# Kernel tuning notes

Measured on AMD Instinct MI355X. Metric: run time of the kernel, lower is better.

## Reference

```python
import jax, jax.numpy as jnp
import numpy as np

HIDDEN = 2048
N_HEADS = 16
HEAD_DIM = HIDDEN // N_HEADS  # 128
GROUP_SIZE = 128
ROPE_THETA = 10000.0
EPS = 1e-8
THRESH = 0.5


def ternary_quantize_groupwise(w):
    O, I = w.shape
    wg = w.reshape(O, I // GROUP_SIZE, GROUP_SIZE)
    scale = jnp.maximum(jnp.mean(jnp.abs(wg), axis=-1, keepdims=True), EPS)
    wn = wg / scale
    q = jnp.where(wn > THRESH, 1.0, jnp.where(wn < -THRESH, -1.0, 0.0))
    return (q * scale).reshape(O, I)


def quantize_with_ste(w):
    wq = ternary_quantize_groupwise(w)
    return w + jax.lax.stop_gradient(wq - w)


def rope_tables(seqlen):
    half = HEAD_DIM // 2
    inv_freq = 1.0 / (ROPE_THETA ** (jnp.arange(half, dtype=jnp.float32) / half))
    freqs = jnp.arange(seqlen, dtype=jnp.float32)[:, None] * inv_freq[None, :]  # [S, half]
    return jnp.cos(freqs), jnp.sin(freqs)


def apply_rope(x, cos, sin):
    # x: [B, H, S, D]; cos/sin: [S, D/2]
    d = x.shape[-1]
    x1, x2 = x[..., : d // 2], x[..., d // 2:]
    c = cos[None, None, :, :].astype(x.dtype)
    s = sin[None, None, :, :].astype(x.dtype)
    return jnp.concatenate([x1 * c - x2 * s, x1 * s + x2 * c], axis=-1)


def setup_inputs() -> dict:
    key = jax.random.key(0)
    ks = jax.random.split(key, 5)
    B, S = 1, 2048
    hidden_states = jax.random.normal(ks[0], (B, S, HIDDEN), dtype=jnp.float32)
    attention_mask = jnp.ones((B, S), dtype=jnp.int32)
    init_scale = 1.0 / np.sqrt(HIDDEN)
    wq = jax.random.normal(ks[1], (HIDDEN, HIDDEN), dtype=jnp.float32) * init_scale
    wk = jax.random.normal(ks[2], (HIDDEN, HIDDEN), dtype=jnp.float32) * init_scale
    wv = jax.random.normal(ks[3], (HIDDEN, HIDDEN), dtype=jnp.float32) * init_scale
    wo = jax.random.normal(ks[4], (HIDDEN, HIDDEN), dtype=jnp.float32) * init_scale
    return {"hidden_states": hidden_states, "attention_mask": attention_mask,
            "wq": wq, "wk": wk, "wv": wv, "wo": wo}


def reference(hidden_states, attention_mask, wq, wk, wv, wo):
    B, S, _ = hidden_states.shape
    cos, sin = rope_tables(S)

    def proj(x, w):
        w_q = quantize_with_ste(w)
        y = jnp.einsum('bsi,oi->bso', x, w_q)
        return y.reshape(B, S, N_HEADS, HEAD_DIM).transpose(0, 2, 1, 3)  # [B,H,S,D]

    q = apply_rope(proj(hidden_states, wq), cos, sin)
    k = apply_rope(proj(hidden_states, wk), cos, sin)
    v = proj(hidden_states, wv)

    scores = jnp.einsum('bhsd,bhtd->bhst', q, k) / np.sqrt(HEAD_DIM)
    causal = jnp.triu(jnp.ones((S, S), dtype=bool), k=1)
    scores = jnp.where(causal[None, None, :, :], -jnp.inf, scores)
    pad = (attention_mask == 0)[:, None, None, :]
    scores = jnp.where(pad, -jnp.inf, scores)

    probs = jax.nn.softmax(scores, axis=-1)
    out = jnp.einsum('bhst,bhtd->bhsd', probs, v)
    out = out.transpose(0, 2, 1, 3).reshape(B, S, HIDDEN)

    wo_q = quantize_with_ste(wo)
    return jnp.einsum('bso,po->bsp', out, wo_q)
```

## Files before the change

### kernel.cpp

```cpp
#include <hip/hip_runtime.h>
#include <cstdint>
#include <cstddef>


typedef __attribute__((ext_vector_type(8))) short bf16x8;
typedef __attribute__((ext_vector_type(4))) float f32x4;
typedef __attribute__((address_space(3))) void lds_void;
typedef const __attribute__((address_space(1))) void gmem_void;

__device__ __forceinline__ short f2bf(float x) {
    union { float f; uint32_t u; } c; c.f = x;
    uint32_t r = (c.u + 0x7FFFu + ((c.u >> 16) & 1u)) >> 16;
    return (short)r;
}
__device__ __forceinline__ float bf2f(short x) {
    union { uint32_t u; float f; } c; c.u = ((uint32_t)(uint16_t)x) << 16;
    return c.f;
}

__global__ __launch_bounds__(64) void zero_flag(int* f) {
    if (threadIdx.x == 0) *f = 0;
}

__global__ __launch_bounds__(256) void detect_kernel(
    const unsigned short* __restrict__ p, int n, int* __restrict__ flag)
{
    int tid = blockIdx.x * 256 + threadIdx.x;
    int cnt = 0;
    for (int i = tid; i < n; i += 65536) {
        int e = (p[i] >> 7) & 0xFF;
        cnt += (e >= 0xF0) ? 1 : 0;
    }
#pragma unroll
    for (int off = 1; off < 64; off <<= 1) cnt += __shfl_xor(cnt, off);
    if ((threadIdx.x & 63) == 0 && cnt) atomicAdd(flag, cnt);
}

__global__ __launch_bounds__(256) void convert_kernel(
    const void* __restrict__ in, short* __restrict__ out, int n,
    const int* __restrict__ flag)
{
    bool isf32 = (*flag > 1000);
    int i = (blockIdx.x * 256 + threadIdx.x) * 4;
    if (i >= n) return;
    if (isf32) {
        float4 v = *(const float4*)((const float*)in + i);
        short4 o;
        o.x = f2bf(v.x); o.y = f2bf(v.y); o.z = f2bf(v.z); o.w = f2bf(v.w);
        *(short4*)(out + i) = o;
    } else {
        *(short4*)(out + i) = *(const short4*)((const short*)in + i);
    }
}

__global__ __launch_bounds__(256) void quant_kernel(
    const void* __restrict__ w0, const void* __restrict__ w1,
    const void* __restrict__ w2, const void* __restrict__ w3,
    short* __restrict__ q0, short* __restrict__ q1,
    short* __restrict__ q2, short* __restrict__ q3,
    const int* __restrict__ flag)
{
    bool isf32 = (*flag > 1000);
    int gw   = blockIdx.x * 4 + (threadIdx.x >> 6);
    int lane = threadIdx.x & 63;
    int mat  = gw >> 15;
    int g    = gw & 32767;
    const void* w = (mat == 0) ? w0 : (mat == 1) ? w1 : (mat == 2) ? w2 : w3;
    short*      q = (mat == 0) ? q0 : (mat == 1) ? q1 : (mat == 2) ? q2 : q3;
    int idx = g * 64 + lane;
    float a, b;
    if (isf32) {
        const float* wf = (const float*)w;
        a = wf[idx * 2]; b = wf[idx * 2 + 1];
    } else {
        int pr = ((const int*)w)[idx];
        a = bf2f((short)(pr & 0xFFFF));
        b = bf2f((short)(((uint32_t)pr) >> 16));
    }
    float s = fabsf(a) + fabsf(b);
#pragma unroll
    for (int off = 1; off < 64; off <<= 1) s += __shfl_xor(s, off);
    float scale = fmaxf(s * (1.0f / 128.0f), 1e-8f);
    float na = a / scale, nb = b / scale;
    float ra = (na > 0.5f) ? scale : (na < -0.5f) ? -scale : 0.0f;
    float rb = (nb > 0.5f) ? scale : (nb < -0.5f) ? -scale : 0.0f;
    ((int*)q)[idx] = (int)(uint16_t)f2bf(ra) | ((int)(uint16_t)f2bf(rb) << 16);
}

__global__ __launch_bounds__(256, 2) void gemm_qkv(
    const short* __restrict__ A, const short* __restrict__ B,
    short* __restrict__ C)
{
    __shared__ short lds[30720];

    int wg = blockIdx.y * 32 + blockIdx.x;
    int sw = (wg & 7) * 64 + (wg >> 3);
    int bx = sw & 31, by = sw >> 5;

    const short* Ab = A + (long long)by * 128 * 2048;
    const short* Bb = B + (long long)bx * 192 * 2048;

    int tid = threadIdx.x, lane = tid & 63, wid = tid >> 6;
    int wr = wid >> 1, wc = wid & 1;
    int quad = lane >> 4, lm = lane & 15;

    f32x4 acc[4][6];
#pragma unroll
    for (int i = 0; i < 4; i++)
#pragma unroll
        for (int j = 0; j < 6; j++)
#pragma unroll
            for (int r = 0; r < 4; r++) acc[i][j][r] = 0.0f;

    auto stage = [&](int tn, short* buf) {
        short* dA = buf;
        short* dB = buf + 4096;
#pragma unroll
        for (int l = 0; l < 2; l++) {
            int ci  = l * 256 + tid;
            int row = ci >> 2;
            int kc  = ((ci & 3) - (row >> 1)) & 3;
            const short* gp = Ab + (long long)row * 2048 + tn * 32 + kc * 8;
            __builtin_amdgcn_global_load_lds((gmem_void*)gp, (lds_void*)(dA + ci * 8), 16, 0, 0);
        }
#pragma unroll
        for (int l = 0; l < 3; l++) {
            int ci  = l * 256 + tid;
            int row = ci >> 2;
            int kc  = ((ci & 3) - (row >> 1)) & 3;
            const short* gp = Bb + (long long)row * 2048 + tn * 32 + kc * 8;
            __builtin_amdgcn_global_load_lds((gmem_void*)gp, (lds_void*)(dB + ci * 8), 16, 0, 0);
        }
    };

    auto tile = [&](short* cur, short* nxt, int tn, bool pf) {
        if (pf) stage(tn, nxt);
        short* cA = cur;
        short* cB = cur + 4096;
        bf16x8 af[4], bg[6];
#pragma unroll
        for (int m = 0; m < 4; m++) {
            int R = wr * 64 + m * 16 + lm;
            af[m] = *(const bf16x8*)(cA + R * 32 + (((quad + (R >> 1)) & 3) << 3));
        }
#pragma unroll
        for (int n = 0; n < 3; n++) {
            int R = wc * 96 + n * 16 + lm;
            bg[n] = *(const bf16x8*)(cB + R * 32 + (((quad + (R >> 1)) & 3) << 3));
        }
        __builtin_amdgcn_s_setprio(1);
#pragma unroll
        for (int m = 0; m < 4; m++)
#pragma unroll
            for (int n = 0; n < 3; n++)
                acc[m][n] = __builtin_amdgcn_mfma_f32_16x16x32_bf16(af[m], bg[n], acc[m][n], 0, 0, 0);
        __builtin_amdgcn_s_setprio(0);
#pragma unroll
        for (int n = 3; n < 6; n++) {
            int R = wc * 96 + n * 16 + lm;
            bg[n] = *(const bf16x8*)(cB + R * 32 + (((quad + (R >> 1)) & 3) << 3));
        }
        __builtin_amdgcn_s_setprio(1);
#pragma unroll
        for (int m = 0; m < 4; m++)
#pragma unroll
            for (int n = 3; n < 6; n++)
                acc[m][n] = __builtin_amdgcn_mfma_f32_16x16x32_bf16(af[m], bg[n], acc[m][n], 0, 0, 0);
        __builtin_amdgcn_s_setprio(0);
        if (pf) asm volatile("s_waitcnt vmcnt(5)" ::: "memory");
        else    asm volatile("s_waitcnt vmcnt(0)" ::: "memory");
        __builtin_amdgcn_s_barrier();
    };

    short* c0 = lds;
    short* c1 = lds + 10240;
    short* c2 = lds + 20480;
    stage(0, c0);
    stage(1, c1);
    asm volatile("s_waitcnt vmcnt(5)" ::: "memory");
    __builtin_amdgcn_s_barrier();

    for (int t = 0; t < 64; t++) {
        tile(c0, c2, t + 2, t + 2 < 64);
        short* tmp = c0; c0 = c1; c1 = c2; c2 = tmp;
    }

#pragma unroll
    for (int m = 0; m < 4; m++)
#pragma unroll
        for (int n = 0; n < 6; n++)
#pragma unroll
            for (int r = 0; r < 4; r++) {
                int row = by * 128 + wr * 64 + m * 16 + quad * 4 + r;
                int col = bx * 192 + wc * 96 + n * 16 + lm;
                C[(long long)row * 6144 + col] = f2bf(acc[m][n][r]);
            }
}

__global__ __launch_bounds__(256) void vtrans_kernel(
    const short* __restrict__ qkv, short* __restrict__ v_t)
{
    __shared__ short lt[4096];
    int bt = blockIdx.x, bo = blockIdx.y;
    int tid = threadIdx.x;
    int r = tid >> 3, c = tid & 7;
#pragma unroll
    for (int h = 0; h < 2; h++) {
        int row = h * 32 + r;
        bf16x8 v = *(const bf16x8*)(qkv + (long long)(bt * 64 + row) * 6144 + 4096 + bo * 64 + c * 8);
        *(bf16x8*)(lt + row * 64 + ((c ^ (row & 7)) << 3)) = v;
    }
    __syncthreads();
#pragma unroll
    for (int h = 0; h < 2; h++) {
        int o = h * 32 + r;
        bf16x8 ov;
#pragma unroll
        for (int k = 0; k < 8; k++) {
            int row = c * 8 + k;
            ov[k] = lt[row * 64 + ((((o >> 3) ^ (row & 7))) << 3) + (o & 7)];
        }
        *(bf16x8*)(v_t + (long long)(bo * 64 + o) * 2048 + bt * 64 + c * 8) = ov;
    }
}

__global__ __launch_bounds__(256) void gemm_wo(
    const short* __restrict__ A, const short* __restrict__ B,
    float* __restrict__ C)
{
    int bx = blockIdx.x, by = blockIdx.y;
    const short* Ab = A + (long long)by * 128 * 2048;
    const short* Bb = B + (long long)bx * 64 * 2048;
    __shared__ short lA[128 * 64];
    __shared__ short lB[64 * 64];
    int tid = threadIdx.x;
    int lane = tid & 63, wv = tid >> 6;
    f32x4 acc[2][4];
#pragma unroll
    for (int i = 0; i < 2; i++)
#pragma unroll
        for (int j = 0; j < 4; j++)
#pragma unroll
            for (int r = 0; r < 4; r++) acc[i][j][r] = 0.0f;

    int rbase = wv * 32;

    for (int k0 = 0; k0 < 2048; k0 += 64) {
        __syncthreads();
#pragma unroll
        for (int i = 0; i < 4; i++) {
            int ci  = i * 256 + tid;
            int row = ci >> 3;
            int kcG = (ci & 7) ^ (row & 7);
            const short* gp = Ab + (long long)row * 2048 + k0 + kcG * 8;
            __builtin_amdgcn_global_load_lds((gmem_void*)gp, (lds_void*)(lA + ci * 8), 16, 0, 0);
        }
#pragma unroll
        for (int i = 0; i < 2; i++) {
            int ci  = i * 256 + tid;
            int row = ci >> 3;
            int kcG = (ci & 7) ^ (row & 7);
            const short* gp = Bb + (long long)row * 2048 + k0 + kcG * 8;
            __builtin_amdgcn_global_load_lds((gmem_void*)gp, (lds_void*)(lB + ci * 8), 16, 0, 0);
        }
        __syncthreads();
#pragma unroll
        for (int kk = 0; kk < 2; kk++) {
            int kc = kk * 4 + (lane >> 4);
            bf16x8 a[2], b[4];
#pragma unroll
            for (int t = 0; t < 2; t++) {
                int r = rbase + t * 16 + (lane & 15);
                a[t] = *(const bf16x8*)(lA + (r * 8 + (kc ^ (r & 7))) * 8);
            }
#pragma unroll
            for (int t = 0; t < 4; t++) {
                int r = t * 16 + (lane & 15);
                b[t] = *(const bf16x8*)(lB + (r * 8 + (kc ^ (r & 7))) * 8);
            }
#pragma unroll
            for (int mt = 0; mt < 2; mt++)
#pragma unroll
                for (int nt = 0; nt < 4; nt++)
                    acc[mt][nt] = __builtin_amdgcn_mfma_f32_16x16x32_bf16(a[mt], b[nt], acc[mt][nt], 0, 0, 0);
        }
    }

    int rq = (lane >> 4) * 4, cq = lane & 15;
#pragma unroll
    for (int mt = 0; mt < 2; mt++)
#pragma unroll
        for (int nt = 0; nt < 4; nt++)
#pragma unroll
            for (int r = 0; r < 4; r++) {
                int row = by * 128 + rbase + mt * 16 + rq + r;
                int col = bx * 64 + nt * 16 + cq;
                C[(long long)row * 2048 + col] = acc[mt][nt][r];
            }
}

__global__ __launch_bounds__(256) void rope_kernel(
    const short* __restrict__ qk,
    short* __restrict__ qr, short* __restrict__ kr)
{
    int idx = blockIdx.x * 256 + threadIdx.x;
    int d = idx & 63;
    int h = (idx >> 6) & 15;
    int s = idx >> 10;
    float inv = exp2f((float)d * -0.20762050593261719f);
    float ang = (float)s * inv;
    float sn, c;
    sincosf(ang, &sn, &c);
    long long io = (long long)s * 6144 + h * 128 + d;
    long long oo = (long long)h * 262144 + (long long)s * 128 + d;
    float x1 = bf2f(qk[io]), x2 = bf2f(qk[io + 64]);
    qr[oo]      = f2bf(x1 * c - x2 * sn);
    qr[oo + 64] = f2bf(x1 * sn + x2 * c);
    x1 = bf2f(qk[io + 2048]); x2 = bf2f(qk[io + 2112]);
    kr[oo]      = f2bf(x1 * c - x2 * sn);
    kr[oo + 64] = f2bf(x1 * sn + x2 * c);
}

__global__ __launch_bounds__(256) void flash_kernel(
    const short* __restrict__ q_r, const short* __restrict__ k_r,
    const short* __restrict__ v_t, float* __restrict__ Opart,
    float* __restrict__ mpart, float* __restrict__ lpart)
{
    const float SC = 0.08838834764831845f;
    int bid = blockIdx.x;
    int qt = 31 - (bid >> 5);
    int h  = (bid >> 1) & 15;
    int z  = bid & 1;
    int n  = qt + 1;
    int jhalf = (n + 1) >> 1;
    int jb = z ? jhalf : 0;
    int je = z ? n : jhalf;

    int tid = threadIdx.x, lane = tid & 63, wv = tid >> 6;
    int quad = lane >> 4, lm = lane & 15;

    __shared__ short lK[64 * 128];
    __shared__ short lV[128 * 64];
    __shared__ short lP[64 * 64];

    const short* qb = q_r + h * 262144 + (qt * 64 + wv * 16) * 128;
    const short* kb = k_r + h * 262144;
    const short* vb = v_t + h * 128 * 2048;

    bf16x8 aq[4];
#pragma unroll
    for (int kc = 0; kc < 4; kc++)
        aq[kc] = *(const bf16x8*)(qb + lm * 128 + kc * 32 + quad * 8);

    f32x4 ao[8];
#pragma unroll
    for (int nt = 0; nt < 8; nt++)
#pragma unroll
        for (int r = 0; r < 4; r++) ao[nt][r] = 0.0f;
    float mrow[4], lrow[4];
#pragma unroll
    for (int r = 0; r < 4; r++) { mrow[r] = -1e30f; lrow[r] = 0.0f; }

    if (jb < je) {
#pragma unroll
        for (int i = 0; i < 4; i++) {
            int ci = i * 256 + tid;
            int r = ci >> 4, cp = ci & 15;
            int c = (cp & 8) | ((cp & 7) ^ (r & 7));
            const short* gp = kb + (jb * 64 + r) * 128 + c * 8;
            __builtin_amdgcn_global_load_lds((gmem_void*)gp, (lds_void*)(lK + ci * 8), 16, 0, 0);
        }
    }
    __syncthreads();

    for (int jt = jb; jt < je; jt++) {
#pragma unroll
        for (int i = 0; i < 4; i++) {
            int ci = i * 256 + tid;
            int r = ci >> 3, cp = ci & 7;
            int c = cp ^ (r & 7);
            const short* gp = vb + r * 2048 + jt * 64 + c * 8;
            __builtin_amdgcn_global_load_lds((gmem_void*)gp, (lds_void*)(lV + ci * 8), 16, 0, 0);
        }
        f32x4 as[4];
#pragma unroll
        for (int nt = 0; nt < 4; nt++)
#pragma unroll
            for (int r = 0; r < 4; r++) as[nt][r] = 0.0f;
#pragma unroll
        for (int kc = 0; kc < 4; kc++) {
#pragma unroll
            for (int nt = 0; nt < 4; nt++) {
                int r = nt * 16 + lm;
                int c = kc * 4 + quad;
                int slot = (c & 8) | ((c & 7) ^ (r & 7));
                bf16x8 bk = *(const bf16x8*)(lK + (r * 16 + slot) * 8);
                as[nt] = __builtin_amdgcn_mfma_f32_16x16x32_bf16(aq[kc], bk, as[nt], 0, 0, 0);
            }
        }
        bool diag = (jt == qt);
#pragma unroll
        for (int nt = 0; nt < 4; nt++)
#pragma unroll
            for (int r = 0; r < 4; r++) {
                float s = as[nt][r] * SC;
                if (diag) {
                    int qg = wv * 16 + quad * 4 + r;
                    int tg = nt * 16 + lm;
                    if (tg > qg) s = -1e30f;
                }
                as[nt][r] = s;
            }
#pragma unroll
        for (int r = 0; r < 4; r++) {
            float mx = fmaxf(fmaxf(as[0][r], as[1][r]), fmaxf(as[2][r], as[3][r]));
#pragma unroll
            for (int off = 1; off < 16; off <<= 1) mx = fmaxf(mx, __shfl_xor(mx, off));
            float mnew = fmaxf(mrow[r], mx);
            float alpha = __expf(mrow[r] - mnew);
            mrow[r] = mnew;
            float psum = 0.0f;
#pragma unroll
            for (int nt = 0; nt < 4; nt++) {
                float p = __expf(as[nt][r] - mnew);
                as[nt][r] = p;
                psum += p;
            }
#pragma unroll
            for (int off = 1; off < 16; off <<= 1) psum += __shfl_xor(psum, off);
            lrow[r] = lrow[r] * alpha + psum;
#pragma unroll
            for (int nt = 0; nt < 8; nt++) ao[nt][r] *= alpha;
            int row = wv * 16 + quad * 4 + r;
#pragma unroll
            for (int nt = 0; nt < 4; nt++) {
                int slot = (nt * 2 + (lm >> 3) + 2 * quad) & 7;
                lP[row * 64 + slot * 8 + (lm & 7)] = f2bf(as[nt][r]);
            }
        }
        __syncthreads();
        if (jt + 1 < je) {
#pragma unroll
            for (int i = 0; i < 4; i++) {
                int ci = i * 256 + tid;
                int r = ci >> 4, cp = ci & 15;
                int c = (cp & 8) | ((cp & 7) ^ (r & 7));
                const short* gp = kb + ((jt + 1) * 64 + r) * 128 + c * 8;
                __builtin_amdgcn_global_load_lds((gmem_void*)gp, (lds_void*)(lK + ci * 8), 16, 0, 0);
            }
        }
#pragma unroll
        for (int kt = 0; kt < 2; kt++) {
            int prow = wv * 16 + lm;
            int slot = (kt * 4 + quad + 2 * (lm >> 2)) & 7;
            bf16x8 ap = *(const bf16x8*)(lP + prow * 64 + slot * 8);
#pragma unroll
            for (int nt = 0; nt < 8; nt++) {
                int r = nt * 16 + lm;
                int c = kt * 4 + quad;
                int vslot = c ^ (r & 7);
                bf16x8 bv = *(const bf16x8*)(lV + (r * 8 + vslot) * 8);
                ao[nt] = __builtin_amdgcn_mfma_f32_16x16x32_bf16(ap, bv, ao[nt], 0, 0, 0);
            }
        }
        __syncthreads();
    }
    float* Ob = Opart + (long long)z * 4194304;
#pragma unroll
    for (int r = 0; r < 4; r++) {
        int sg = qt * 64 + wv * 16 + quad * 4 + r;
#pragma unroll
        for (int nt = 0; nt < 8; nt++) {
            int dg = h * 128 + nt * 16 + lm;
            Ob[(long long)sg * 2048 + dg] = ao[nt][r];
        }
        if (lm == 0) {
            mpart[z * 32768 + h * 2048 + sg] = mrow[r];
            lpart[z * 32768 + h * 2048 + sg] = lrow[r];
        }
    }
}

__global__ __launch_bounds__(256) void combine_kernel(
    const float* __restrict__ O0, const float* __restrict__ O1,
    const float* __restrict__ mpart, const float* __restrict__ lpart,
    short* __restrict__ attn)
{
    int idx = blockIdx.x * 256 + threadIdx.x;
    int e = idx * 4;
    int s = e >> 11, h = (e & 2047) >> 7;
    float m0 = mpart[h * 2048 + s], m1 = mpart[32768 + h * 2048 + s];
    float l0 = lpart[h * 2048 + s], l1 = lpart[32768 + h * 2048 + s];
    float M = fmaxf(m0, m1);
    float w0 = __expf(m0 - M), w1 = __expf(m1 - M);
    float inv = 1.0f / (l0 * w0 + l1 * w1);
    float4 a = *(const float4*)(O0 + e);
    float4 b = *(const float4*)(O1 + e);
    short4 o;
    o.x = f2bf((a.x * w0 + b.x * w1) * inv);
    o.y = f2bf((a.y * w0 + b.y * w1) * inv);
    o.z = f2bf((a.z * w0 + b.z * w1) * inv);
    o.w = f2bf((a.w * w0 + b.w * w1) * inv);
    *(short4*)(attn + e) = o;
}

extern "C" void kernel_launch(void* const* d_in, const int* in_sizes, int n_in,
                              void* d_out, int out_size, void* d_ws, size_t ws_size,
                              hipStream_t stream)
{
    const void* x  = d_in[0];
    const void* wq = d_in[2];
    const void* wk = d_in[3];
    const void* wv = d_in[4];
    const void* wo = d_in[5];

    char* ws = (char*)d_ws;
    size_t off = 0;
    auto alloc = [&](size_t b) { void* p = ws + off; off += (b + 255) & ~(size_t)255; return p; };
    short* wqkv_q = (short*)alloc(25165824);
    short* wo_q   = (short*)alloc(8388608);
    float* Opart  = (float*)alloc(33554432);
    short* qkv    = (short*)Opart;
    short* v_t    = (short*)alloc(8388608);
    short* q_r    = (short*)alloc(8388608);
    short* k_r    = (short*)alloc(8388608);
    short* attn   = (short*)alloc(8388608);
    short* x_bf   = (short*)alloc(8388608);
    float* mpart  = (float*)alloc(262144);
    float* lpart  = (float*)alloc(262144);
    int*   flag   = (int*)alloc(256);
    if (off > ws_size) return;

    zero_flag<<<1, 64, 0, stream>>>(flag);
    detect_kernel<<<256, 256, 0, stream>>>(
        (const unsigned short*)x, in_sizes[0], flag);
    convert_kernel<<<4096, 256, 0, stream>>>(x, x_bf, 4194304, flag);

    quant_kernel<<<32768, 256, 0, stream>>>(wq, wk, wv, wo,
        wqkv_q, wqkv_q + 4194304, wqkv_q + 8388608, wo_q, flag);

    gemm_qkv<<<dim3(32, 16), 256, 0, stream>>>(x_bf, wqkv_q, qkv);

    rope_kernel<<<8192, 256, 0, stream>>>(qkv, q_r, k_r);
    vtrans_kernel<<<dim3(32, 32), 256, 0, stream>>>(qkv, v_t);

    flash_kernel<<<1024, 256, 0, stream>>>(q_r, k_r, v_t, Opart, mpart, lpart);
    combine_kernel<<<4096, 256, 0, stream>>>(
        Opart, Opart + 4194304, mpart, lpart, attn);

    gemm_wo<<<dim3(32, 16), 256, 0, stream>>>(attn, wo_q, (float*)d_out);
}
```

Measured before the change: 315.3 us.

## Pipeline gemm_wo with triple-buffered LDS and vectorize quant and rope kernels

gemm_wo is rebuilt as a triple-buffered pipeline with a 32-wide K step. Global-to-LDS loads are prefetched two tiles ahead, with waitcnt/barrier sync, a swizzled workgroup order and a 2x2 wave layout, so memory latency overlaps with MFMA work. The quant kernel now handles 4 elements per thread with vector loads and a 32-lane shuffle reduction, and multiplies by a reciprocal instead of dividing. The rope kernel handles 8 elements per thread with 16-byte vector loads and stores. These cut launch width and memory transactions, but the hand-written vmcnt counts and the changed division rounding add correctness risk.

Measured after the change: 310.1 us. Within noise of the previous version (-1.6%).

```diff
diff --git a/kernel.cpp b/kernel.cpp
--- a/kernel.cpp
+++ b/kernel.cpp
@@ -61,30 +61,31 @@
     const int* __restrict__ flag)
 {
     bool isf32 = (*flag > 1000);
-    int gw   = blockIdx.x * 4 + (threadIdx.x >> 6);
-    int lane = threadIdx.x & 63;
-    int mat  = gw >> 15;
-    int g    = gw & 32767;
+    int t   = blockIdx.x * 256 + threadIdx.x;
+    int mat = t >> 20;
+    int e4  = t & 1048575;
     const void* w = (mat == 0) ? w0 : (mat == 1) ? w1 : (mat == 2) ? w2 : w3;
     short*      q = (mat == 0) ? q0 : (mat == 1) ? q1 : (mat == 2) ? q2 : q3;
-    int idx = g * 64 + lane;
-    float a, b;
+    float a0, a1, a2, a3;
     if (isf32) {
-        const float* wf = (const float*)w;
-        a = wf[idx * 2]; b = wf[idx * 2 + 1];
+        float4 v = *(const float4*)((const float*)w + (long long)e4 * 4);
+        a0 = v.x; a1 = v.y; a2 = v.z; a3 = v.w;
     } else {
-        int pr = ((const int*)w)[idx];
-        a = bf2f((short)(pr & 0xFFFF));
-        b = bf2f((short)(((uint32_t)pr) >> 16));
-    }
-    float s = fabsf(a) + fabsf(b);
-#pragma unroll
-    for (int off = 1; off < 64; off <<= 1) s += __shfl_xor(s, off);
+        short4 v = *(const short4*)((const short*)w + (long long)e4 * 4);
+        a0 = bf2f(v.x); a1 = bf2f(v.y); a2 = bf2f(v.z); a3 = bf2f(v.w);
+    }
+    float s = fabsf(a0) + fabsf(a1) + fabsf(a2) + fabsf(a3);
+#pragma unroll
+    for (int off = 1; off < 32; off <<= 1) s += __shfl_xor(s, off);
     float scale = fmaxf(s * (1.0f / 128.0f), 1e-8f);
-    float na = a / scale, nb = b / scale;
-    float ra = (na > 0.5f) ? scale : (na < -0.5f) ? -scale : 0.0f;
-    float rb = (nb > 0.5f) ? scale : (nb < -0.5f) ? -scale : 0.0f;
-    ((int*)q)[idx] = (int)(uint16_t)f2bf(ra) | ((int)(uint16_t)f2bf(rb) << 16);
+    float inv = 1.0f / scale;
+    auto qz = [&](float a) -> short {
+        float na = a * inv;
+        return f2bf((na > 0.5f) ? scale : (na < -0.5f) ? -scale : 0.0f);
+    };
+    short4 o;
+    o.x = qz(a0); o.y = qz(a1); o.z = qz(a2); o.w = qz(a3);
+    *(short4*)(q + (long long)e4 * 4) = o;
 }
 
 __global__ __launch_bounds__(256, 2) void gemm_qkv(
@@ -224,78 +225,100 @@
     }
 }
 
-__global__ __launch_bounds__(256) void gemm_wo(
+__global__ __launch_bounds__(256, 2) void gemm_wo(
     const short* __restrict__ A, const short* __restrict__ B,
     float* __restrict__ C)
 {
-    int bx = blockIdx.x, by = blockIdx.y;
+    __shared__ short lds[18432];
+
+    int wg = blockIdx.y * 32 + blockIdx.x;
+    int sw = (wg & 7) * 64 + (wg >> 3);
+    int bx = sw & 31, by = sw >> 5;
+
     const short* Ab = A + (long long)by * 128 * 2048;
     const short* Bb = B + (long long)bx * 64 * 2048;
-    __shared__ short lA[128 * 64];
-    __shared__ short lB[64 * 64];
-    int tid = threadIdx.x;
-    int lane = tid & 63, wv = tid >> 6;
-    f32x4 acc[2][4];
-#pragma unroll
-    for (int i = 0; i < 2; i++)
-#pragma unroll
-        for (int j = 0; j < 4; j++)
+
+    int tid = threadIdx.x, lane = tid & 63, wid = tid >> 6;
+    int wr = wid >> 1, wc = wid & 1;
+    int quad = lane >> 4, lm = lane & 15;
+
+    f32x4 acc[4][2];
+#pragma unroll
+    for (int i = 0; i < 4; i++)
+#pragma unroll
+        for (int j = 0; j < 2; j++)
 #pragma unroll
             for (int r = 0; r < 4; r++) acc[i][j][r] = 0.0f;
 
-    int rbase = wv * 32;
-
-    for (int k0 = 0; k0 < 2048; k0 += 64) {
-        __syncthreads();
-#pragma unroll
-        for (int i = 0; i < 4; i++) {
-            int ci  = i * 256 + tid;
-            int row = ci >> 3;
-            int kcG = (ci & 7) ^ (row & 7);
-            const short* gp = Ab + (long long)row * 2048 + k0 + kcG * 8;
-            __builtin_amdgcn_global_load_lds((gmem_void*)gp, (lds_void*)(lA + ci * 8), 16, 0, 0);
-        }
-#pragma unroll
-        for (int i = 0; i < 2; i++) {
-            int ci  = i * 256 + tid;
-            int row = ci >> 3;
-            int kcG = (ci & 7) ^ (row & 7);
-            const short* gp = Bb + (long long)row * 2048 + k0 + kcG * 8;
-            __builtin_amdgcn_global_load_lds((gmem_void*)gp, (lds_void*)(lB + ci * 8), 16, 0, 0);
-        }
-        __syncthreads();
-#pragma unroll
-        for (int kk = 0; kk < 2; kk++) {
-            int kc = kk * 4 + (lane >> 4);
-            bf16x8 a[2], b[4];
-#pragma unroll
-            for (int t = 0; t < 2; t++) {
-                int r = rbase + t * 16 + (lane & 15);
-                a[t] = *(const bf16x8*)(lA + (r * 8 + (kc ^ (r & 7))) * 8);
-            }
-#pragma unroll
-            for (int t = 0; t < 4; t++) {
-                int r = t * 16 + (lane & 15);
-                b[t] = *(const bf16x8*)(lB + (r * 8 + (kc ^ (r & 7))) * 8);
-            }
-#pragma unroll
-            for (int mt = 0; mt < 2; mt++)
-#pragma unroll
-                for (int nt = 0; nt < 4; nt++)
-                    acc[mt][nt] = __builtin_amdgcn_mfma_f32_16x16x32_bf16(a[mt], b[nt], acc[mt][nt], 0, 0, 0);
-        }
-    }
-
-    int rq = (lane >> 4) * 4, cq = lane & 15;
-#pragma unroll
-    for (int mt = 0; mt < 2; mt++)
-#pragma unroll
-        for (int nt = 0; nt < 4; nt++)
+    auto stage = [&](int tn, short* buf) {
+        short* dA = buf;
+        short* dB = buf + 4096;
+#pragma unroll
+        for (int l = 0; l < 2; l++) {
+            int ci  = l * 256 + tid;
+            int row = ci >> 2;
+            int kc  = ((ci & 3) - (row >> 1)) & 3;
+            const short* gp = Ab + (long long)row * 2048 + tn * 32 + kc * 8;
+            __builtin_amdgcn_global_load_lds((gmem_void*)gp, (lds_void*)(dA + ci * 8), 16, 0, 0);
+        }
+        {
+            int ci  = tid;
+            int row = ci >> 2;
+            int kc  = ((ci & 3) - (row >> 1)) & 3;
+            const short* gp = Bb + (long long)row * 2048 + tn * 32 + kc * 8;
+            __builtin_amdgcn_global_load_lds((gmem_void*)gp, (lds_void*)(dB + ci * 8), 16, 0, 0);
+        }
+    };
+
+    auto tile = [&](short* cur, short* nxt, int tn, bool pf) {
+        if (pf) stage(tn, nxt);
+        short* cA = cur;
+        short* cB = cur + 4096;
+        bf16x8 af[4], bg[2];
+#pragma unroll
+        for (int m = 0; m < 4; m++) {
+            int R = wr * 64 + m * 16 + lm;
+            af[m] = *(const bf16x8*)(cA + R * 32 + (((quad + (R >> 1)) & 3) << 3));
+        }
+#pragma unroll
+        for (int n = 0; n < 2; n++) {
+            int R = wc * 32 + n * 16 + lm;
+            bg[n] = *(const bf16x8*)(cB + R * 32 + (((quad + (R >> 1)) & 3) << 3));
+        }
+        __builtin_amdgcn_s_setprio(1);
+#pragma unroll
+        for (int m = 0; m < 4; m++)
+#pragma unroll
+            for (int n = 0; n < 2; n++)
+                acc[m][n] = __builtin_amdgcn_mfma_f32_16x16x32_bf16(af[m], bg[n], acc[m][n], 0, 0, 0);
+        __builtin_amdgcn_s_setprio(0);
+        if (pf) asm volatile("s_waitcnt vmcnt(3)" ::: "memory");
+        else    asm volatile("s_waitcnt vmcnt(0)" ::: "memory");
+        __builtin_amdgcn_s_barrier();
+    };
+
+    short* c0 = lds;
+    short* c1 = lds + 6144;
+    short* c2 = lds + 12288;
+    stage(0, c0);
+    stage(1, c1);
+    asm volatile("s_waitcnt vmcnt(3)" ::: "memory");
+    __builtin_amdgcn_s_barrier();
+
+    for (int t = 0; t < 64; t++) {
+        tile(c0, c2, t + 2, t + 2 < 64);
+        short* tmp = c0; c0 = c1; c1 = c2; c2 = tmp;
+    }
+
+#pragma unroll
+    for (int m = 0; m < 4; m++)
+#pragma unroll
+        for (int n = 0; n < 2; n++)
 #pragma unroll
             for (int r = 0; r < 4; r++) {
-                int row = by * 128 + rbase + mt * 16 + rq + r;
-                int col = bx * 64 + nt * 16 + cq;
-                C[(long long)row * 2048 + col] = acc[mt][nt][r];
+                int row = by * 128 + wr * 64 + m * 16 + quad * 4 + r;
+                int col = bx * 64 + wc * 32 + n * 16 + lm;
+                C[(long long)row * 2048 + col] = acc[m][n][r];
             }
 }
 
@@ -304,21 +327,33 @@
     short* __restrict__ qr, short* __restrict__ kr)
 {
     int idx = blockIdx.x * 256 + threadIdx.x;
-    int d = idx & 63;
-    int h = (idx >> 6) & 15;
-    int s = idx >> 10;
-    float inv = exp2f((float)d * -0.20762050593261719f);
-    float ang = (float)s * inv;
-    float sn, c;
-    sincosf(ang, &sn, &c);
-    long long io = (long long)s * 6144 + h * 128 + d;
-    long long oo = (long long)h * 262144 + (long long)s * 128 + d;
-    float x1 = bf2f(qk[io]), x2 = bf2f(qk[io + 64]);
-    qr[oo]      = f2bf(x1 * c - x2 * sn);
-    qr[oo + 64] = f2bf(x1 * sn + x2 * c);
-    x1 = bf2f(qk[io + 2048]); x2 = bf2f(qk[io + 2112]);
-    kr[oo]      = f2bf(x1 * c - x2 * sn);
-    kr[oo + 64] = f2bf(x1 * sn + x2 * c);
+    int d8 = (idx & 7) * 8;
+    int h  = (idx >> 3) & 15;
+    int s  = idx >> 7;
+    long long io = (long long)s * 6144 + h * 128 + d8;
+    long long oo = (long long)h * 262144 + (long long)s * 128 + d8;
+    bf16x8 x1q = *(const bf16x8*)(qk + io);
+    bf16x8 x2q = *(const bf16x8*)(qk + io + 64);
+    bf16x8 x1k = *(const bf16x8*)(qk + io + 2048);
+    bf16x8 x2k = *(const bf16x8*)(qk + io + 2112);
+    bf16x8 o1q, o2q, o1k, o2k;
+#pragma unroll
+    for (int j = 0; j < 8; j++) {
+        float inv = exp2f((float)(d8 + j) * -0.20762050593261719f);
+        float ang = (float)s * inv;
+        float sn, c;
+        sincosf(ang, &sn, &c);
+        float a1 = bf2f(x1q[j]), a2 = bf2f(x2q[j]);
+        o1q[j] = f2bf(a1 * c - a2 * sn);
+        o2q[j] = f2bf(a1 * sn + a2 * c);
+        float b1 = bf2f(x1k[j]), b2 = bf2f(x2k[j]);
+        o1k[j] = f2bf(b1 * c - b2 * sn);
+        o2k[j] = f2bf(b1 * sn + b2 * c);
+    }
+    *(bf16x8*)(qr + oo)      = o1q;
+    *(bf16x8*)(qr + oo + 64) = o2q;
+    *(bf16x8*)(kr + oo)      = o1k;
+    *(bf16x8*)(kr + oo + 64) = o2k;
 }
 
 __global__ __launch_bounds__(256) void flash_kernel(
@@ -536,12 +571,12 @@
         (const unsigned short*)x, in_sizes[0], flag);
     convert_kernel<<<4096, 256, 0, stream>>>(x, x_bf, 4194304, flag);
 
-    quant_kernel<<<32768, 256, 0, stream>>>(wq, wk, wv, wo,
+    quant_kernel<<<16384, 256, 0, stream>>>(wq, wk, wv, wo,
         wqkv_q, wqkv_q + 4194304, wqkv_q + 8388608, wo_q, flag);
 
     gemm_qkv<<<dim3(32, 16), 256, 0, stream>>>(x_bf, wqkv_q, qkv);
 
-    rope_kernel<<<8192, 256, 0, stream>>>(qkv, q_r, k_r);
+    rope_kernel<<<1024, 256, 0, stream>>>(qkv, q_r, k_r);
     vtrans_kernel<<<dim3(32, 32), 256, 0, stream>>>(qkv, v_t);
 
     flash_kernel<<<1024, 256, 0, stream>>>(q_r, k_r, v_t, Opart, mpart, lpart);
```
